# Performance work log

Hardware: AMD Instinct MI355X
Metric: run time of the kernel (lower is better)

The kernel has to match this reference:

```python
import jax, jax.numpy as jnp
import numpy as np

N_TOKENS = 8192
NQ = 6
NL = 2


def ry_mat(theta):
    # theta: scalar or (B,) -> (2,2) or (B,2,2) complex RY matrix
    c = jnp.cos(theta / 2)
    s = jnp.sin(theta / 2)
    return jnp.stack([jnp.stack([c, -s], -1), jnp.stack([s, c], -1)], -2).astype(jnp.complex64)


def apply_1q(state, gate, q, nq):
    # state: (B, 2**nq); gate: (2,2) shared or (B,2,2) per-batch
    B = state.shape[0]
    st = state.reshape(B, 2 ** q, 2, -1)
    if gate.ndim == 3:
        st = jnp.einsum('bij,bajc->baic', gate, st)
    else:
        st = jnp.einsum('ij,bajc->baic', gate, st)
    return st.reshape(B, -1)


def apply_rz(state, theta, q, nq):
    # diagonal RZ: multiply phases, no matmul needed
    B = state.shape[0]
    st = state.reshape(B, 2 ** q, 2, -1)
    ph = jnp.stack([jnp.exp(-0.5j * theta), jnp.exp(0.5j * theta)]).astype(jnp.complex64)
    return (st * ph[None, None, :, None]).reshape(B, -1)


def apply_cnot(state, c, t, nq):
    B = state.shape[0]
    st = state.reshape((B,) + (2,) * nq)
    s0 = jnp.take(st, 0, axis=1 + c)
    s1 = jnp.take(st, 1, axis=1 + c)
    ta = 1 + t - (1 if t > c else 0)  # target axis after removing control axis
    s1 = jnp.flip(s1, axis=ta)
    st = jnp.stack([s0, s1], axis=1 + c)
    return st.reshape(B, -1)


def prepare_states(x, params, nl, nq):
    # x: (B, nq) angles; params: (nl, nq, 2). Returns (B, 2**nq) complex statevectors.
    B = x.shape[0]
    state = jnp.zeros((B, 2 ** nq), jnp.complex64).at[:, 0].set(1.0)
    for q in range(nq):  # RY angle embedding
        state = apply_1q(state, ry_mat(x[:, q]), q, nq)
    for l in range(nl):  # PQC layers: RY, RZ rotations + CNOT ring
        for q in range(nq):
            state = apply_1q(state, ry_mat(params[l, q, 0]), q, nq)
            state = apply_rz(state, params[l, q, 1], q, nq)
        for q in range(nq):
            state = apply_cnot(state, q, (q + 1) % nq, nq)
    return state


def setup_inputs() -> dict:
    key = jax.random.key(0)
    k1, k2, k3, k4 = jax.random.split(key, 4)
    return {
        'x_tokens': jax.random.normal(k1, (N_TOKENS, NQ), dtype=jnp.float32),
        'params_q': 0.1 * jax.random.normal(k2, (NL, NQ, 2), dtype=jnp.float32),
        'params_k': 0.1 * jax.random.normal(k3, (NL, NQ, 2), dtype=jnp.float32),
        'params_v': 0.1 * jax.random.normal(k4, (NL, NQ, 2), dtype=jnp.float32),
    }


def reference(x_tokens, params_q, params_k, params_v):
    nq = x_tokens.shape[1]
    nl = params_q.shape[0]
    sq = prepare_states(x_tokens, params_q, nl, nq)  # (N, 2**nq)
    sk = prepare_states(x_tokens, params_k, nl, nq)
    ov = jnp.einsum('id,jd->ij', sq, jnp.conj(sk))  # pairwise overlaps (N, N)
    logits = jnp.real(ov * jnp.conj(ov))            # swap-test fidelity |<q|k>|^2
    attn = jax.nn.softmax(logits, axis=-1)
    sv = prepare_states(x_tokens, params_v, nl, nq)
    probs = jnp.real(sv * jnp.conj(sv))             # (N, 2**nq)
    idx = jnp.arange(2 ** nq)
    bits = (idx[None, :] >> (nq - 1 - jnp.arange(nq))[:, None]) & 1  # (nq, 2**nq)
    signs = (1.0 - 2.0 * bits).astype(probs.dtype)
    V = probs @ signs.T                              # <Z_q> per qubit -> (N, nq)
    return attn @ V
```

## Files before the change

### kernel.cpp

```cpp
#include <hip/hip_runtime.h>
#include <hip/hip_bf16.h>

#define NT 8192
#define NQB 6
#define NL 2
#define JSPLIT 16
#define JSLICE (NT / JSPLIT)
#define CHUNK 64
#define NCHUNK (JSLICE / CHUNK)
#define IPW 32
#define WPB 4
#define IPB (IPW * WPB)
#define NBI (NT / IPB)

typedef __bf16 bf16x8 __attribute__((ext_vector_type(8)));
typedef float f32x4 __attribute__((ext_vector_type(4)));

static __device__ __forceinline__ unsigned int pack_bf2(float a, float b) {
  unsigned short lo = __builtin_bit_cast(unsigned short, __float2bfloat16(a));
  unsigned short hi = __builtin_bit_cast(unsigned short, __float2bfloat16(b));
  return (unsigned int)lo | ((unsigned int)hi << 16);
}

static __device__ __forceinline__ int cnot_src(int p, int q) {
  const int mc = 1 << (5 - q);
  const int mt = 1 << (5 - ((q + 1) % NQB));
  return (p & mc) ? (p ^ mt) : p;
}

__global__ __launch_bounds__(256) void prep_kernel(
    const float* __restrict__ x, const float* __restrict__ pq,
    const float* __restrict__ pk, const float* __restrict__ pv,
    unsigned int* __restrict__ Are, unsigned int* __restrict__ Bk,
    float4* __restrict__ V4)
{
  const int wid  = blockIdx.x * 4 + (threadIdx.x >> 6);
  const int lane = threadIdx.x & 63;
  const int set  = wid >> 13;
  const int tok  = wid & (NT - 1);
  const float* pp = (set == 0) ? pq : ((set == 1) ? pk : pv);

  int m = lane;
#pragma unroll
  for (int q = 5; q >= 0; --q) m = cnot_src(m, q);
  int inv = lane;
#pragma unroll
  for (int q = 0; q < 6; ++q) inv = cnot_src(inv, q);

  float R = 1.f, phi = 0.f;
#pragma unroll
  for (int q = 0; q < 6; ++q) {
    float s, c;
    __sincosf(0.5f * (x[tok * NQB + q] + pp[q * 2 + 0]), &s, &c);
    const float bh = 0.5f * pp[q * 2 + 1];
    if ((m >> (5 - q)) & 1) { R *= s; phi += bh; }
    else                    { R *= c; phi -= bh; }
  }
  float sp, cp;
  __sincosf(phi, &sp, &cp);
  float re = R * cp, im = R * sp;

#pragma unroll
  for (int q = 0; q < 6; ++q) {
    const int mask = 1 << (5 - q);
    float s, c;
    __sincosf(0.5f * pp[2 * NQB + q * 2 + 0], &s, &c);
    const float pre = __shfl_xor(re, mask, 64);
    const float pim = __shfl_xor(im, mask, 64);
    const float se = (lane & mask) ? s : -s;
    re = fmaf(se, pre, c * re);
    im = fmaf(se, pim, c * im);
  }
  float phi2 = 0.f;
#pragma unroll
  for (int q = 0; q < 6; ++q) {
    const float bh = 0.5f * pp[2 * NQB + q * 2 + 1];
    phi2 += (lane & (1 << (5 - q))) ? bh : -bh;
  }
  float s2, c2;
  __sincosf(phi2, &s2, &c2);
  const float fre = re * c2 - im * s2;
  const float fim = re * s2 + im * c2;

  if (set == 0) {
    Are[tok * 64 + inv] = pack_bf2(fre, fim);
  } else if (set == 1) {
    Bk[tok * 64 + inv] = pack_bf2(fre, fim);
  } else {
    const float prob = fre * fre + fim * fim;
    float vq[NQB];
#pragma unroll
    for (int q = 0; q < NQB; ++q) {
      float v = (inv & (1 << (5 - q))) ? -prob : prob;
#pragma unroll
      for (int off = 1; off < 64; off <<= 1) v += __shfl_xor(v, off, 64);
      vq[q] = v;
    }
    if (lane == 0) {
      V4[tok * 2 + 0] = make_float4(vq[0], vq[1], vq[2], vq[3]);
      V4[tok * 2 + 1] = make_float4(vq[4], vq[5], 0.f, 0.f);
    }
  }
}

__global__ __launch_bounds__(256, 2) void attn_kernel(
    const uint4* __restrict__ Are, const uint4* __restrict__ Bk,
    const float4* __restrict__ V4, float* __restrict__ part)
{
  __shared__ uint4 kbuf[CHUNK * 17];
  __shared__ float4 vbuf[CHUNK * 2];

  const int tid  = threadIdx.x;
  const int lane = tid & 63;
  const int wave = tid >> 6;
  const int col  = lane & 15;
  const int quad = lane >> 4;

  const int ib = blockIdx.x & (NBI - 1);
  const int js = blockIdx.x / NBI;
  const int ibase = ib * IPB + wave * IPW;
  const int jbase0 = js * JSLICE;

  bf16x8 aRe[2][4], aIm[2][4];
#pragma unroll
  for (int rt = 0; rt < 2; ++rt) {
    const int row = ibase + rt * 16 + col;
    const uint4* pr = Are + row * 16 + quad;
#pragma unroll
    for (int s = 0; s < 4; ++s) {
      const uint4 u = pr[s * 4];
      uint4 w;
      w.x = ((u.x << 16) | (u.x >> 16)) ^ 0x80000000u;
      w.y = ((u.y << 16) | (u.y >> 16)) ^ 0x80000000u;
      w.z = ((u.z << 16) | (u.z >> 16)) ^ 0x80000000u;
      w.w = ((u.w << 16) | (u.w >> 16)) ^ 0x80000000u;
      aRe[rt][s] = __builtin_bit_cast(bf16x8, u);
      aIm[rt][s] = __builtin_bit_cast(bf16x8, w);
    }
  }

  float den[8];
  float num[8][6];
#pragma unroll
  for (int r = 0; r < 8; ++r) {
    den[r] = 0.f;
#pragma unroll
    for (int q = 0; q < 6; ++q) num[r][q] = 0.f;
  }

#pragma unroll 1
  for (int c = 0; c < NCHUNK; ++c) {
    const int jb = jbase0 + c * CHUNK;
    __syncthreads();
#pragma unroll
    for (int r = 0; r < 4; ++r) {
      const int idx = r * 256 + tid;
      kbuf[(idx >> 4) * 17 + (idx & 15)] = Bk[(jb + (idx >> 4)) * 16 + (idx & 15)];
    }
    if (tid < 2 * CHUNK) vbuf[tid] = V4[jb * 2 + tid];
    __syncthreads();

#pragma unroll
    for (int ct = 0; ct < 4; ++ct) {
      const int keyl = ct * 16 + col;
      bf16x8 bfr[4];
#pragma unroll
      for (int s = 0; s < 4; ++s)
        bfr[s] = __builtin_bit_cast(bf16x8, kbuf[keyl * 17 + s * 4 + quad]);
      const float4 v01 = vbuf[keyl * 2 + 0];
      const float4 v23 = vbuf[keyl * 2 + 1];
      const float vv[6] = {v01.x, v01.y, v01.z, v01.w, v23.x, v23.y};
#pragma unroll
      for (int rt = 0; rt < 2; ++rt) {
        f32x4 aR = {0.f, 0.f, 0.f, 0.f};
        f32x4 aI = {0.f, 0.f, 0.f, 0.f};
#pragma unroll
        for (int s = 0; s < 4; ++s) {
          aR = __builtin_amdgcn_mfma_f32_16x16x32_bf16(aRe[rt][s], bfr[s], aR, 0, 0, 0);
          aI = __builtin_amdgcn_mfma_f32_16x16x32_bf16(aIm[rt][s], bfr[s], aI, 0, 0, 0);
        }
#pragma unroll
        for (int r = 0; r < 4; ++r) {
          const float f = aR[r] * aR[r] + aI[r] * aI[r];
          const float w = __expf(f);
          const int rr = rt * 4 + r;
          den[rr] += w;
#pragma unroll
          for (int q = 0; q < 6; ++q) num[rr][q] = fmaf(w, vv[q], num[rr][q]);
        }
      }
    }
  }

#pragma unroll
  for (int rr = 0; rr < 8; ++rr) {
#pragma unroll
    for (int off = 1; off < 16; off <<= 1) {
      den[rr] += __shfl_xor(den[rr], off, 64);
#pragma unroll
      for (int q = 0; q < 6; ++q) num[rr][q] += __shfl_xor(num[rr][q], off, 64);
    }
  }

  if (col == 0) {
#pragma unroll
    for (int rt = 0; rt < 2; ++rt) {
#pragma unroll
      for (int r = 0; r < 4; ++r) {
        const int row = ibase + rt * 16 + quad * 4 + r;
        float* p = part + ((size_t)(js * NT + row)) * 8;
        const int rr = rt * 4 + r;
#pragma unroll
        for (int q = 0; q < 6; ++q) p[q] = num[rr][q];
        p[6] = den[rr];
      }
    }
  }
}

__global__ __launch_bounds__(256) void combine_kernel(
    const float* __restrict__ part, float* __restrict__ out)
{
  const int row = blockIdx.x * 256 + threadIdx.x;
  float acc[7] = {0.f, 0.f, 0.f, 0.f, 0.f, 0.f, 0.f};
#pragma unroll
  for (int js = 0; js < JSPLIT; ++js) {
    const float* p = part + ((size_t)(js * NT + row)) * 8;
#pragma unroll
    for (int q = 0; q < 7; ++q) acc[q] += p[q];
  }
  const float inv = 1.0f / acc[6];
#pragma unroll
  for (int q = 0; q < 6; ++q)
    out[row * 6 + q] = acc[q] * inv;
}

extern "C" void kernel_launch(void* const* d_in, const int* in_sizes, int n_in,
                              void* d_out, int out_size, void* d_ws, size_t ws_size,
                              hipStream_t stream) {
  const float* x  = (const float*)d_in[0];
  const float* pq = (const float*)d_in[1];
  const float* pk = (const float*)d_in[2];
  const float* pv = (const float*)d_in[3];
  char* ws = (char*)d_ws;
  unsigned int* Are = (unsigned int*)(ws);
  unsigned int* Bk  = (unsigned int*)(ws + (size_t)(2u << 20));
  float*        V   = (float*)(ws + (size_t)(4u << 20));
  float*        prt = (float*)(ws + (size_t)(4u << 20) + (size_t)(256u << 10));

  prep_kernel<<<(NT * 3) / 4, 256, 0, stream>>>(x, pq, pk, pv, Are, Bk, (float4*)V);
  attn_kernel<<<NBI * JSPLIT, 256, 0, stream>>>((const uint4*)Are, (const uint4*)Bk,
                                                (const float4*)V, prt);
  combine_kernel<<<NT / 256, 256, 0, stream>>>(prt, (float*)d_out);
}
```

Before: 129.2 us.

## Compute attention-weighted V sum with MFMA and async double-buffered key loads

The per-element FMA accumulation of exp weights times six V values is replaced by a second MFMA. The weights are packed to fp16 in per-wave LDS and multiplied against a transposed fp16 V matrix. V is stored as a hi/lo fp16 split to keep precision, and a ones column yields the denominator. Keys switch from bf16 to fp16, are XOR-swizzled in global memory, and are staged into LDS with global_load_lds double buffering. Tiles shrink to 16 rows per wave and 32-key chunks. The trade is fp16 range and precision risk on weights that can reach about e^1, plus more barriers per chunk.

```diff
diff --git a/kernel.cpp b/kernel.cpp
--- a/kernel.cpp
+++ b/kernel.cpp
@@ -1,24 +1,26 @@
 #include <hip/hip_runtime.h>
 #include <hip/hip_bf16.h>
+#include <hip/hip_fp16.h>
 
 #define NT 8192
 #define NQB 6
 #define NL 2
 #define JSPLIT 16
 #define JSLICE (NT / JSPLIT)
-#define CHUNK 64
+#define CHUNK 32
 #define NCHUNK (JSLICE / CHUNK)
-#define IPW 32
+#define IPW 16
 #define WPB 4
 #define IPB (IPW * WPB)
 #define NBI (NT / IPB)
-
-typedef __bf16 bf16x8 __attribute__((ext_vector_type(8)));
+#define WSTRIDE 40
+
+typedef _Float16 f16x8 __attribute__((ext_vector_type(8)));
 typedef float f32x4 __attribute__((ext_vector_type(4)));
 
-static __device__ __forceinline__ unsigned int pack_bf2(float a, float b) {
-  unsigned short lo = __builtin_bit_cast(unsigned short, __float2bfloat16(a));
-  unsigned short hi = __builtin_bit_cast(unsigned short, __float2bfloat16(b));
+static __device__ __forceinline__ unsigned int pack_h2(float a, float b) {
+  unsigned short lo = __builtin_bit_cast(unsigned short, (_Float16)a);
+  unsigned short hi = __builtin_bit_cast(unsigned short, (_Float16)b);
   return (unsigned int)lo | ((unsigned int)hi << 16);
 }
 
@@ -28,11 +30,16 @@
   return (p & mc) ? (p ^ mt) : p;
 }
 
+#define GLOAD_LDS16(g, l)                                      \
+  __builtin_amdgcn_global_load_lds(                            \
+      (const __attribute__((address_space(1))) void*)(g),      \
+      (__attribute__((address_space(3))) void*)(l), 16, 0, 0)
+
 __global__ __launch_bounds__(256) void prep_kernel(
     const float* __restrict__ x, const float* __restrict__ pq,
     const float* __restrict__ pk, const float* __restrict__ pv,
     unsigned int* __restrict__ Are, unsigned int* __restrict__ Bk,
-    float4* __restrict__ V4)
+    unsigned short* __restrict__ Vt)
 {
   const int wid  = blockIdx.x * 4 + (threadIdx.x >> 6);
   const int lane = threadIdx.x & 63;
@@ -83,9 +90,10 @@
   const float fim = re * s2 + im * c2;
 
   if (set == 0) {
-    Are[tok * 64 + inv] = pack_bf2(fre, fim);
+    Are[tok * 64 + inv] = pack_h2(fre, fim);
   } else if (set == 1) {
-    Bk[tok * 64 + inv] = pack_bf2(fre, fim);
+    const int sidx = ((((inv >> 2) ^ (tok & 15)) << 2) | (inv & 3));
+    Bk[tok * 64 + sidx] = pack_h2(fre, fim);
   } else {
     const float prob = fre * fre + fim * fim;
     float vq[NQB];
@@ -96,19 +104,34 @@
       for (int off = 1; off < 64; off <<= 1) v += __shfl_xor(v, off, 64);
       vq[q] = v;
     }
-    if (lane == 0) {
-      V4[tok * 2 + 0] = make_float4(vq[0], vq[1], vq[2], vq[3]);
-      V4[tok * 2 + 1] = make_float4(vq[4], vq[5], 0.f, 0.f);
+    if (lane < 16) {
+      const int q = lane & 7;
+      float sel = vq[0];
+      if (q == 1) sel = vq[1];
+      if (q == 2) sel = vq[2];
+      if (q == 3) sel = vq[3];
+      if (q == 4) sel = vq[4];
+      if (q == 5) sel = vq[5];
+      if (q == 6) sel = 1.0f;
+      if (q == 7) sel = 0.0f;
+      float outv;
+      if (lane < 8) {
+        outv = sel;
+      } else {
+        const float hi = (float)(_Float16)sel;
+        outv = (q < 6) ? (sel - hi) : 0.0f;
+      }
+      Vt[lane * NT + tok] = __builtin_bit_cast(unsigned short, (_Float16)outv);
     }
   }
 }
 
 __global__ __launch_bounds__(256, 2) void attn_kernel(
     const uint4* __restrict__ Are, const uint4* __restrict__ Bk,
-    const float4* __restrict__ V4, float* __restrict__ part)
+    const unsigned short* __restrict__ Vt, float* __restrict__ part)
 {
-  __shared__ uint4 kbuf[CHUNK * 17];
-  __shared__ float4 vbuf[CHUNK * 2];
+  __shared__ uint4 kbuf[2][CHUNK * 16];
+  __shared__ __align__(16) unsigned short wbuf[WPB][16][WSTRIDE];
 
   const int tid  = threadIdx.x;
   const int lane = tid & 63;
@@ -117,15 +140,13 @@
   const int quad = lane >> 4;
 
   const int ib = blockIdx.x & (NBI - 1);
-  const int js = blockIdx.x / NBI;
+  const int js = blockIdx.x >> 7;
   const int ibase = ib * IPB + wave * IPW;
   const int jbase0 = js * JSLICE;
 
-  bf16x8 aRe[2][4], aIm[2][4];
-#pragma unroll
-  for (int rt = 0; rt < 2; ++rt) {
-    const int row = ibase + rt * 16 + col;
-    const uint4* pr = Are + row * 16 + quad;
+  f16x8 qRe[4], qIm[4];
+  {
+    const uint4* pr = Are + (ibase + col) * 16 + quad;
 #pragma unroll
     for (int s = 0; s < 4; ++s) {
       const uint4 u = pr[s * 4];
@@ -134,87 +155,73 @@
       w.y = ((u.y << 16) | (u.y >> 16)) ^ 0x80000000u;
       w.z = ((u.z << 16) | (u.z >> 16)) ^ 0x80000000u;
       w.w = ((u.w << 16) | (u.w >> 16)) ^ 0x80000000u;
-      aRe[rt][s] = __builtin_bit_cast(bf16x8, u);
-      aIm[rt][s] = __builtin_bit_cast(bf16x8, w);
-    }
-  }
-
-  float den[8];
-  float num[8][6];
-#pragma unroll
-  for (int r = 0; r < 8; ++r) {
-    den[r] = 0.f;
-#pragma unroll
-    for (int q = 0; q < 6; ++q) num[r][q] = 0.f;
-  }
+      qRe[s] = __builtin_bit_cast(f16x8, u);
+      qIm[s] = __builtin_bit_cast(f16x8, w);
+    }
+  }
+
+  int koff[4];
+#pragma unroll
+  for (int s = 0; s < 4; ++s) koff[s] = (((s * 4 + quad) ^ col) << 4);
+
+  f32x4 acc = {0.f, 0.f, 0.f, 0.f};
+
+  auto stage = [&](int buf, int c) {
+#pragma unroll
+    for (int r = 0; r < 2; ++r) {
+      const int slot = wave * 2 + r;
+      GLOAD_LDS16(Bk + (size_t)(jbase0 + c * CHUNK) * 16 + slot * 64 + lane,
+                  &kbuf[buf][slot * 64]);
+    }
+  };
+
+  stage(0, 0);
 
 #pragma unroll 1
   for (int c = 0; c < NCHUNK; ++c) {
+    const int cur = c & 1;
     const int jb = jbase0 + c * CHUNK;
-    __syncthreads();
-#pragma unroll
-    for (int r = 0; r < 4; ++r) {
-      const int idx = r * 256 + tid;
-      kbuf[(idx >> 4) * 17 + (idx & 15)] = Bk[(jb + (idx >> 4)) * 16 + (idx & 15)];
-    }
-    if (tid < 2 * CHUNK) vbuf[tid] = V4[jb * 2 + tid];
-    __syncthreads();
-
-#pragma unroll
-    for (int ct = 0; ct < 4; ++ct) {
-      const int keyl = ct * 16 + col;
-      bf16x8 bfr[4];
-#pragma unroll
-      for (int s = 0; s < 4; ++s)
-        bfr[s] = __builtin_bit_cast(bf16x8, kbuf[keyl * 17 + s * 4 + quad]);
-      const float4 v01 = vbuf[keyl * 2 + 0];
-      const float4 v23 = vbuf[keyl * 2 + 1];
-      const float vv[6] = {v01.x, v01.y, v01.z, v01.w, v23.x, v23.y};
-#pragma unroll
-      for (int rt = 0; rt < 2; ++rt) {
-        f32x4 aR = {0.f, 0.f, 0.f, 0.f};
-        f32x4 aI = {0.f, 0.f, 0.f, 0.f};
-#pragma unroll
-        for (int s = 0; s < 4; ++s) {
-          aR = __builtin_amdgcn_mfma_f32_16x16x32_bf16(aRe[rt][s], bfr[s], aR, 0, 0, 0);
-          aI = __builtin_amdgcn_mfma_f32_16x16x32_bf16(aIm[rt][s], bfr[s], aI, 0, 0, 0);
-        }
-#pragma unroll
-        for (int r = 0; r < 4; ++r) {
-          const float f = aR[r] * aR[r] + aI[r] * aI[r];
-          const float w = __expf(f);
-          const int rr = rt * 4 + r;
-          den[rr] += w;
-#pragma unroll
-          for (int q = 0; q < 6; ++q) num[rr][q] = fmaf(w, vv[q], num[rr][q]);
-        }
+    const f16x8 vb = *(const f16x8*)(Vt + (size_t)col * NT + jb + quad * 8);
+    if (c + 1 < NCHUNK) {
+      stage(cur ^ 1, c + 1);
+      asm volatile("s_waitcnt vmcnt(2)" ::: "memory");
+    } else {
+      asm volatile("s_waitcnt vmcnt(0)" ::: "memory");
+    }
+    __builtin_amdgcn_s_barrier();
+
+#pragma unroll
+    for (int ct = 0; ct < 2; ++ct) {
+      const char* kb = (const char*)kbuf[cur] + (ct * 16 + col) * 256;
+      f16x8 bfr[4];
+#pragma unroll
+      for (int s = 0; s < 4; ++s) bfr[s] = *(const f16x8*)(kb + koff[s]);
+      f32x4 aR = {0.f, 0.f, 0.f, 0.f};
+      f32x4 aI = {0.f, 0.f, 0.f, 0.f};
+#pragma unroll
+      for (int s = 0; s < 4; ++s) {
+        aR = __builtin_amdgcn_mfma_f32_16x16x32_f16(bfr[s], qRe[s], aR, 0, 0, 0);
+        aI = __builtin_amdgcn_mfma_f32_16x16x32_f16(bfr[s], qIm[s], aI, 0, 0, 0);
       }
-    }
-  }
-
-#pragma unroll
-  for (int rr = 0; rr < 8; ++rr) {
-#pragma unroll
-    for (int off = 1; off < 16; off <<= 1) {
-      den[rr] += __shfl_xor(den[rr], off, 64);
-#pragma unroll
-      for (int q = 0; q < 6; ++q) num[rr][q] += __shfl_xor(num[rr][q], off, 64);
-    }
-  }
-
-  if (col == 0) {
-#pragma unroll
-    for (int rt = 0; rt < 2; ++rt) {
-#pragma unroll
-      for (int r = 0; r < 4; ++r) {
-        const int row = ibase + rt * 16 + quad * 4 + r;
-        float* p = part + ((size_t)(js * NT + row)) * 8;
-        const int rr = rt * 4 + r;
-#pragma unroll
-        for (int q = 0; q < 6; ++q) p[q] = num[rr][q];
-        p[6] = den[rr];
-      }
-    }
+      const float w0 = __expf(aR[0] * aR[0] + aI[0] * aI[0]);
+      const float w1 = __expf(aR[1] * aR[1] + aI[1] * aI[1]);
+      const float w2 = __expf(aR[2] * aR[2] + aI[2] * aI[2]);
+      const float w3 = __expf(aR[3] * aR[3] + aI[3] * aI[3]);
+      *(uint2*)&wbuf[wave][col][ct * 16 + quad * 4] =
+          make_uint2(pack_h2(w0, w1), pack_h2(w2, w3));
+    }
+    const f16x8 wA = *(const f16x8*)&wbuf[wave][col][quad * 8];
+    acc = __builtin_amdgcn_mfma_f32_16x16x32_f16(wA, vb, acc, 0, 0, 0);
+    __builtin_amdgcn_s_barrier();
+  }
+
+  float res[4];
+#pragma unroll
+  for (int r = 0; r < 4; ++r) res[r] = acc[r] + __shfl_xor(acc[r], 8, 64);
+  if (col < 8) {
+    float* p = part + ((size_t)(js * NT + ibase + quad * 4)) * 8 + col;
+#pragma unroll
+    for (int r = 0; r < 4; ++r) p[r * 8] = res[r];
   }
 }
 
@@ -243,13 +250,13 @@
   const float* pk = (const float*)d_in[2];
   const float* pv = (const float*)d_in[3];
   char* ws = (char*)d_ws;
-  unsigned int* Are = (unsigned int*)(ws);
-  unsigned int* Bk  = (unsigned int*)(ws + (size_t)(2u << 20));
-  float*        V   = (float*)(ws + (size_t)(4u << 20));
-  float*        prt = (float*)(ws + (size_t)(4u << 20) + (size_t)(256u << 10));
-
-  prep_kernel<<<(NT * 3) / 4, 256, 0, stream>>>(x, pq, pk, pv, Are, Bk, (float4*)V);
+  unsigned int*   Are = (unsigned int*)(ws);
+  unsigned int*   Bk  = (unsigned int*)(ws + (size_t)(2u << 20));
+  unsigned short* Vt  = (unsigned short*)(ws + (size_t)(4u << 20));
+  float*          prt = (float*)(ws + (size_t)(4u << 20) + (size_t)(256u << 10));
+
+  prep_kernel<<<(NT * 3) / 4, 256, 0, stream>>>(x, pq, pk, pv, Are, Bk, Vt);
   attn_kernel<<<NBI * JSPLIT, 256, 0, stream>>>((const uint4*)Are, (const uint4*)Bk,
-                                                (const float4*)V, prt);
+                                                Vt, prt);
   combine_kernel<<<NT / 256, 256, 0, stream>>>(prt, (float*)d_out);
 }
```

Result: no change. 131.7 us (+1.9%).
